# Kernel optimization log

Measured on AMD Instinct MI355X. Metric: run time of the kernel, lower is better.

## Reference

```python
import jax, jax.numpy as jnp
import numpy as np

B, S, IN, H = 16, 1024, 1024, 1024

def setup_inputs() -> dict:
    key = jax.random.key(0)
    k1, k2 = jax.random.split(key)
    x = jax.random.normal(k1, (B, S, IN), dtype=jnp.float32)
    # xavier_uniform with gain sqrt(2) over shape [2H, IN]
    limit = np.sqrt(2.0) * np.sqrt(6.0 / (2 * H + IN))
    W = jax.random.uniform(k2, (2 * H, IN), dtype=jnp.float32, minval=-limit, maxval=limit)
    return {"x": x, "W": W}

def reference(x, W):
    # i = x @ W.T -> [B, S, 2H]; split into key/value pre-activations
    i = jnp.einsum('bsi,oi->bso', x, W)
    ik, iv = jnp.split(i, 2, axis=2)          # each [B, S, H]
    mem0 = jnp.zeros((x.shape[0], H, H), dtype=x.dtype)

    def step(mem, kv):
        ik_t, iv_t = kv                        # [B, H] each
        k = jax.nn.relu(ik_t)
        v = jax.nn.relu(iv_t)
        # Hebbian plasticity rule: delta_mem = key outer val
        mem = mem + jnp.einsum('bk,bv->bkv', k, v)
        return mem, (k, v)

    # scan over time: move seq axis to front
    kv_seq = (jnp.swapaxes(ik, 0, 1), jnp.swapaxes(iv, 0, 1))  # [S, B, H]
    mem, (keys, vals) = jax.lax.scan(step, mem0, kv_seq)
    keys = jnp.swapaxes(keys, 0, 1)            # [B, S, H]
    vals = jnp.swapaxes(vals, 0, 1)
    return mem, keys, vals
```

## Files before the change

### kernel.cpp

```cpp
#include <hip/hip_runtime.h>

#define B_  16
#define S_  1024
#define IN_ 1024
#define H_  1024
#define N1  (2*H_)
#define M1  (B_*S_)
#define K1  IN_
#define XN  (M1*IN_)
#define WN  (N1*IN_)
#define LDG 1024

#define BM  256
#define BN  256
#define BK  64
#define CP  257

typedef __attribute__((ext_vector_type(8))) short  short8;
typedef __attribute__((ext_vector_type(4))) float  floatx4;

__device__ __forceinline__ unsigned short f2bf(float f) {
    unsigned int u = __float_as_uint(f);
    u += 0x7fffu + ((u >> 16) & 1u);
    return (unsigned short)(u >> 16);
}

#define GLDS16(gp, lp) __builtin_amdgcn_global_load_lds(                      \
    (const __attribute__((address_space(1))) void*)(gp),                      \
    (__attribute__((address_space(3))) void*)(lp), 16, 0, 0)

__global__ __launch_bounds__(256) void convert_kernel(
    const float* __restrict__ x, const float* __restrict__ W,
    unsigned short* __restrict__ xb, unsigned short* __restrict__ Wb)
{
    size_t i = ((size_t)blockIdx.x * 256 + threadIdx.x) * 8;
    const float* src;
    unsigned short* dst;
    if (i < (size_t)XN) { src = x + i; dst = xb + i; }
    else                { src = W + (i - XN); dst = Wb + (i - XN); }
    float4 a = *(const float4*)(src);
    float4 b = *(const float4*)(src + 4);
    ushort4 p = { f2bf(a.x), f2bf(a.y), f2bf(a.z), f2bf(a.w) };
    ushort4 q = { f2bf(b.x), f2bf(b.y), f2bf(b.z), f2bf(b.w) };
    *(ushort4*)(dst)     = p;
    *(ushort4*)(dst + 4) = q;
}

__device__ __forceinline__ void stage_unit(
    const unsigned short* Ag, const unsigned short* Bg,
    unsigned short* lbuf, int u, int kt, int wave, int lane)
{
    const unsigned short* src = (u < 2) ? (Ag + (size_t)u * 128 * LDG)
                                        : (Bg + (size_t)(u - 2) * 128 * LDG);
    unsigned short* dstu = lbuf + ((u < 2) ? u * 8192 : 16384 + (u - 2) * 8192);
#pragma unroll
    for (int h = 0; h < 2; ++h) {
        int e   = (wave * 2 + h) * 64 + lane;
        int row = e >> 3, c = e & 7;
        int cs  = c ^ (row & 7);
        GLDS16(src + (size_t)row * LDG + kt + cs * 8, dstu + (wave * 2 + h) * 512);
    }
}

__device__ __forceinline__ void gemm_core(
    const unsigned short* Ag, const unsigned short* Bg,
    unsigned short* lds, floatx4 (&acc)[8][4], int wave, int lane)
{
    const int quad = lane >> 4, r = lane & 15;
    const int wmw  = (wave >> 2) * 128;
    const int wnw  = (wave & 3) * 64;

#pragma unroll
    for (int u = 0; u < 4; ++u) stage_unit(Ag, Bg, lds, u, 0, wave, lane);

    for (int t = 0; t < 16; ++t) {
        unsigned short* bufc = lds + (t & 1) * 32768;
        unsigned short* bufn = lds + ((t + 1) & 1) * 32768;
        const int  ktn = (t + 1) * BK;
        const bool st  = (t < 15);
        __syncthreads();
        const unsigned short* cA = bufc;
        const unsigned short* cB = bufc + 16384;
        short8 bfr[4];
#pragma unroll
        for (int kc = 0; kc < 2; ++kc)
#pragma unroll
        for (int mh = 0; mh < 2; ++mh) {
            const int g = kc * 4 + quad;
            short8 af[4];
#pragma unroll
            for (int i = 0; i < 4; ++i)
                af[i] = *(const short8*)(cA + (wmw + (mh * 4 + i) * 16 + r) * BK
                                            + (g ^ (r & 7)) * 8);
            if (mh == 0) {
#pragma unroll
                for (int j = 0; j < 4; ++j)
                    bfr[j] = *(const short8*)(cB + (wnw + j * 16 + r) * BK
                                                 + (g ^ (r & 7)) * 8);
            }
            if (st) stage_unit(Ag, Bg, bufn, kc * 2 + mh, ktn, wave, lane);
            __builtin_amdgcn_sched_barrier(0);
            __builtin_amdgcn_s_barrier();
            __builtin_amdgcn_s_setprio(1);
#pragma unroll
            for (int i = 0; i < 4; ++i)
#pragma unroll
                for (int j = 0; j < 4; ++j)
                    acc[mh * 4 + i][j] = __builtin_amdgcn_mfma_f32_16x16x32_bf16(
                        af[i], bfr[j], acc[mh * 4 + i][j], 0, 0, 0);
            __builtin_amdgcn_s_setprio(0);
            __builtin_amdgcn_sched_barrier(0);
            if (kc + mh < 2) __builtin_amdgcn_s_barrier();
        }
    }
    __syncthreads();
}

__global__ __launch_bounds__(512, 2) void gemm1_kernel(
    const unsigned short* __restrict__ xb, const unsigned short* __restrict__ Wb,
    float* __restrict__ out,
    unsigned short* __restrict__ kT, unsigned short* __restrict__ vT)
{
    __shared__ unsigned short lds[65536];

    const int tid  = threadIdx.x;
    const int wave = tid >> 6, lane = tid & 63;
    const int quad = lane >> 4, r = lane & 15;
    const int wmw  = (wave >> 2) * 128;
    const int wnw  = (wave & 3) * 64;

    const int L   = blockIdx.x;
    const int xcd = L & 7, s = L >> 3;
    const int mt  = xcd * 8 + (s >> 3);
    const int nt  = s & 7;
    const int m0  = mt * BM, n0 = nt * BN;

    const unsigned short* Ag = xb + (size_t)m0 * K1;
    const unsigned short* Bg = Wb + (size_t)n0 * K1;

    floatx4 acc[8][4] = {};
    gemm_core(Ag, Bg, lds, acc, wave, lane);

    const bool isKeys = (nt < 4);
    float* outKV    = out + (isKeys ? (size_t)M1 * H_ : (size_t)2 * M1 * H_);
    const int ncol0 = isKeys ? n0 : (n0 - 1024);

#pragma unroll
    for (int f = 0; f < 8; ++f)
#pragma unroll
        for (int j = 0; j < 4; ++j)
#pragma unroll
            for (int d = 0; d < 4; ++d) {
                int row_l = wmw + f * 16 + quad * 4 + d;
                int col_l = wnw + j * 16 + r;
                outKV[(size_t)(m0 + row_l) * H_ + ncol0 + col_l] =
                    fmaxf(acc[f][j][d], 0.0f);
            }

    unsigned short* wsT = isKeys ? kT : vT;
    const int b  = m0 >> 10;
    const int s0 = m0 & 1023;
    unsigned short* dstB = wsT + (size_t)b * H_ * S_ + (size_t)ncol0 * S_ + s0;

#pragma unroll
    for (int ch = 0; ch < 2; ++ch) {
        if ((wave >> 2) == ch) {
#pragma unroll
            for (int f = 0; f < 8; ++f)
#pragma unroll
                for (int j = 0; j < 4; ++j)
#pragma unroll
                    for (int d = 0; d < 4; ++d) {
                        int lrow = f * 16 + quad * 4 + d;
                        int col  = wnw + j * 16 + r;
                        lds[lrow * CP + col] = f2bf(fmaxf(acc[f][j][d], 0.0f));
                    }
        }
        __syncthreads();
#pragma unroll
        for (int it = 0; it < 16; ++it) {
            int o   = it * 512 + tid;
            int n_l = o >> 5;
            int m4  = (o & 31) * 4;
            ushort4 v;
            v.x = lds[(m4 + 0) * CP + n_l];
            v.y = lds[(m4 + 1) * CP + n_l];
            v.z = lds[(m4 + 2) * CP + n_l];
            v.w = lds[(m4 + 3) * CP + n_l];
            *(ushort4*)(dstB + (size_t)n_l * S_ + ch * 128 + m4) = v;
        }
        __syncthreads();
    }
}

__global__ __launch_bounds__(512, 2) void gemm2_kernel(
    const unsigned short* __restrict__ kT, const unsigned short* __restrict__ vT,
    float* __restrict__ mem)
{
    __shared__ unsigned short lds[65536];

    const int tid  = threadIdx.x;
    const int wave = tid >> 6, lane = tid & 63;
    const int quad = lane >> 4, r = lane & 15;
    const int wmw  = (wave >> 2) * 128;
    const int wnw  = (wave & 3) * 64;

    const int L   = blockIdx.x;
    const int xcd = L & 7, s = L >> 3;
    const int b   = xcd * 2 + (s >> 4);
    const int tt  = s & 15;
    const int m0  = (tt >> 2) * BM;
    const int n0  = (tt & 3) * BN;

    const unsigned short* Ag = kT + (size_t)b * H_ * S_ + (size_t)m0 * S_;
    const unsigned short* Bg = vT + (size_t)b * H_ * S_ + (size_t)n0 * S_;

    floatx4 acc[8][4] = {};
    gemm_core(Ag, Bg, lds, acc, wave, lane);

    float* outb = mem + (size_t)b * H_ * H_;
#pragma unroll
    for (int f = 0; f < 8; ++f)
#pragma unroll
        for (int j = 0; j < 4; ++j)
#pragma unroll
            for (int d = 0; d < 4; ++d) {
                int row_l = wmw + f * 16 + quad * 4 + d;
                int col_l = wnw + j * 16 + r;
                outb[(size_t)(m0 + row_l) * H_ + n0 + col_l] = acc[f][j][d];
            }
}

extern "C" void kernel_launch(void* const* d_in, const int* in_sizes, int n_in,
                              void* d_out, int out_size, void* d_ws, size_t ws_size,
                              hipStream_t stream) {
    const float* x = (const float*)d_in[0];
    const float* W = (const float*)d_in[1];
    float* out = (float*)d_out;

    unsigned short* xb = (unsigned short*)d_out;
    unsigned short* Wb = xb + (size_t)XN;

    unsigned short* kT = (unsigned short*)d_ws;
    unsigned short* vT = kT + (size_t)B_ * H_ * S_;

    convert_kernel<<<dim3((XN + WN) / 2048), dim3(256), 0, stream>>>(x, W, xb, Wb);

    gemm1_kernel<<<dim3(512), dim3(512), 0, stream>>>(xb, Wb, out, kT, vT);

    gemm2_kernel<<<dim3(256), dim3(512), 0, stream>>>(kT, vT, out);
}
```

Measured before the change: 349.4 us.

## Split GEMM K-tile into halves with vmcnt-gated pipelined staging

Reorganises the LDS tile into two 32-wide K-halves per operand, each with a 4-way XOR swizzle. Synchronisation changes from a full __syncthreads plus extra barriers per iteration to an s_waitcnt vmcnt wait followed by a barrier before each half. The next tile's halves are prefetched while the current half computes, so compute can start as soon as its own half has landed rather than waiting for the whole tile. The risks are weaker bank-conflict avoidance from the narrower swizzle and correctness that depends on exact counts of outstanding loads.

Result: no change. 350.8 us (+0.4%).

```diff
diff --git a/kernel.cpp b/kernel.cpp
--- a/kernel.cpp
+++ b/kernel.cpp
@@ -16,6 +16,10 @@
 #define BK  64
 #define CP  257
 
+#define USZ  8192
+#define ASZ  16384
+#define TBUF 32768
+
 typedef __attribute__((ext_vector_type(8))) short  short8;
 typedef __attribute__((ext_vector_type(4))) float  floatx4;
 
@@ -28,6 +32,10 @@
 #define GLDS16(gp, lp) __builtin_amdgcn_global_load_lds(                      \
     (const __attribute__((address_space(1))) void*)(gp),                      \
     (__attribute__((address_space(3))) void*)(lp), 16, 0, 0)
+
+#define WAITVM(N) { asm volatile("s_waitcnt vmcnt(" #N ")" ::: "memory");     \
+                    __builtin_amdgcn_s_barrier();                             \
+                    __builtin_amdgcn_sched_barrier(0); }
 
 __global__ __launch_bounds__(256) void convert_kernel(
     const float* __restrict__ x, const float* __restrict__ W,
@@ -46,19 +54,50 @@
     *(ushort4*)(dst + 4) = q;
 }
 
-__device__ __forceinline__ void stage_unit(
+__device__ __forceinline__ void stage_u(
     const unsigned short* Ag, const unsigned short* Bg,
-    unsigned short* lbuf, int u, int kt, int wave, int lane)
-{
-    const unsigned short* src = (u < 2) ? (Ag + (size_t)u * 128 * LDG)
-                                        : (Bg + (size_t)(u - 2) * 128 * LDG);
-    unsigned short* dstu = lbuf + ((u < 2) ? u * 8192 : 16384 + (u - 2) * 8192);
+    unsigned short* buf, int op, int kh, int kt, int wave, int lane)
+{
+    const unsigned short* src = op ? Bg : Ag;
+    unsigned short* dst = buf + op * ASZ + kh * USZ;
 #pragma unroll
     for (int h = 0; h < 2; ++h) {
         int e   = (wave * 2 + h) * 64 + lane;
-        int row = e >> 3, c = e & 7;
-        int cs  = c ^ (row & 7);
-        GLDS16(src + (size_t)row * LDG + kt + cs * 8, dstu + (wave * 2 + h) * 512);
+        int row = e >> 2, p = e & 3;
+        int c   = p ^ (row & 3);
+        GLDS16(src + (size_t)row * LDG + kt + kh * 32 + c * 8,
+               dst + (wave * 2 + h) * 512);
+    }
+}
+
+__device__ __forceinline__ void half_tile(
+    const unsigned short* bufc, floatx4 (&acc)[8][4], int kc,
+    const unsigned short* Ag, const unsigned short* Bg,
+    unsigned short* bufn, int ktn, bool st,
+    int wave, int lane, int wmw, int wnw, int quad, int r)
+{
+    const unsigned short* cA = bufc + kc * USZ;
+    const unsigned short* cB = bufc + ASZ + kc * USZ;
+    const int sw = (quad ^ (r & 3)) * 8;
+    short8 bfr[4];
+#pragma unroll
+    for (int j = 0; j < 4; ++j)
+        bfr[j] = *(const short8*)(cB + (wnw + j * 16 + r) * 32 + sw);
+#pragma unroll
+    for (int mh = 0; mh < 2; ++mh) {
+        short8 af[4];
+#pragma unroll
+        for (int i = 0; i < 4; ++i)
+            af[i] = *(const short8*)(cA + (wmw + (mh * 4 + i) * 16 + r) * 32 + sw);
+        if (st) stage_u(Ag, Bg, bufn, mh, kc, ktn, wave, lane);
+        __builtin_amdgcn_s_setprio(1);
+#pragma unroll
+        for (int i = 0; i < 4; ++i)
+#pragma unroll
+            for (int j = 0; j < 4; ++j)
+                acc[mh * 4 + i][j] = __builtin_amdgcn_mfma_f32_16x16x32_bf16(
+                    af[i], bfr[j], acc[mh * 4 + i][j], 0, 0, 0);
+        __builtin_amdgcn_s_setprio(0);
     }
 }
 
@@ -70,48 +109,26 @@
     const int wmw  = (wave >> 2) * 128;
     const int wnw  = (wave & 3) * 64;
 
-#pragma unroll
-    for (int u = 0; u < 4; ++u) stage_unit(Ag, Bg, lds, u, 0, wave, lane);
-
-    for (int t = 0; t < 16; ++t) {
-        unsigned short* bufc = lds + (t & 1) * 32768;
-        unsigned short* bufn = lds + ((t + 1) & 1) * 32768;
-        const int  ktn = (t + 1) * BK;
-        const bool st  = (t < 15);
-        __syncthreads();
-        const unsigned short* cA = bufc;
-        const unsigned short* cB = bufc + 16384;
-        short8 bfr[4];
-#pragma unroll
-        for (int kc = 0; kc < 2; ++kc)
-#pragma unroll
-        for (int mh = 0; mh < 2; ++mh) {
-            const int g = kc * 4 + quad;
-            short8 af[4];
-#pragma unroll
-            for (int i = 0; i < 4; ++i)
-                af[i] = *(const short8*)(cA + (wmw + (mh * 4 + i) * 16 + r) * BK
-                                            + (g ^ (r & 7)) * 8);
-            if (mh == 0) {
-#pragma unroll
-                for (int j = 0; j < 4; ++j)
-                    bfr[j] = *(const short8*)(cB + (wnw + j * 16 + r) * BK
-                                                 + (g ^ (r & 7)) * 8);
-            }
-            if (st) stage_unit(Ag, Bg, bufn, kc * 2 + mh, ktn, wave, lane);
-            __builtin_amdgcn_sched_barrier(0);
-            __builtin_amdgcn_s_barrier();
-            __builtin_amdgcn_s_setprio(1);
-#pragma unroll
-            for (int i = 0; i < 4; ++i)
-#pragma unroll
-                for (int j = 0; j < 4; ++j)
-                    acc[mh * 4 + i][j] = __builtin_amdgcn_mfma_f32_16x16x32_bf16(
-                        af[i], bfr[j], acc[mh * 4 + i][j], 0, 0, 0);
-            __builtin_amdgcn_s_setprio(0);
-            __builtin_amdgcn_sched_barrier(0);
-            if (kc + mh < 2) __builtin_amdgcn_s_barrier();
-        }
+    stage_u(Ag, Bg, lds, 0, 0, 0, wave, lane);
+    stage_u(Ag, Bg, lds, 1, 0, 0, wave, lane);
+    stage_u(Ag, Bg, lds, 0, 1, 0, wave, lane);
+    stage_u(Ag, Bg, lds, 1, 1, 0, wave, lane);
+
+    for (int t = 0; t < 15; ++t) {
+        unsigned short* bufc = lds + (t & 1) * TBUF;
+        unsigned short* bufn = lds + ((t + 1) & 1) * TBUF;
+        const int ktn = (t + 1) * BK;
+        WAITVM(4)
+        half_tile(bufc, acc, 0, Ag, Bg, bufn, ktn, true, wave, lane, wmw, wnw, quad, r);
+        WAITVM(4)
+        half_tile(bufc, acc, 1, Ag, Bg, bufn, ktn, true, wave, lane, wmw, wnw, quad, r);
+    }
+    {
+        unsigned short* bufc = lds + TBUF;
+        WAITVM(4)
+        half_tile(bufc, acc, 0, Ag, Bg, bufc, 0, false, wave, lane, wmw, wnw, quad, r);
+        WAITVM(0)
+        half_tile(bufc, acc, 1, Ag, Bg, bufc, 0, false, wave, lane, wmw, wnw, quad, r);
     }
     __syncthreads();
 }
```

## Shrink GEMM tiles to 128x256 with 3-slot LDS ring and BK=32

Applied to the files above, without the earlier changes.

Both GEMMs switch from 256x256 tiles with BK=64 double buffering to 128x256 tiles with BK=32 and a three-slot LDS ring. Each slot is waited on with explicit vmcnt counters and a single barrier per k-step. Smaller tiles halve accumulator registers and LDS use, aiming for 4 blocks per CU and twice as many workgroups, which improves occupancy and latency hiding. The cost is lower arithmetic intensity per tile and more k-iterations with barrier overhead, and the transpose epilogue now stages the full tile in LDS at once.

New measurement: 365.9 us. 1.05x slower.

```diff
diff --git a/kernel.cpp b/kernel.cpp
--- a/kernel.cpp
+++ b/kernel.cpp
@@ -9,12 +9,12 @@
 #define K1  IN_
 #define XN  (M1*IN_)
 #define WN  (N1*IN_)
-#define LDG 1024
-
-#define BM  256
-#define BN  256
-#define BK  64
-#define CP  257
+
+#define BMr  128
+#define BNr  256
+#define SLOT 12288
+#define RING 36864
+#define CPP  264
 
 typedef __attribute__((ext_vector_type(8))) short  short8;
 typedef __attribute__((ext_vector_type(4))) float  floatx4;
@@ -46,99 +46,88 @@
     *(ushort4*)(dst + 4) = q;
 }
 
-__device__ __forceinline__ void stage_unit(
+__device__ __forceinline__ void stage_ph(
     const unsigned short* Ag, const unsigned short* Bg,
-    unsigned short* lbuf, int u, int kt, int wave, int lane)
-{
-    const unsigned short* src = (u < 2) ? (Ag + (size_t)u * 128 * LDG)
-                                        : (Bg + (size_t)(u - 2) * 128 * LDG);
-    unsigned short* dstu = lbuf + ((u < 2) ? u * 8192 : 16384 + (u - 2) * 8192);
+    unsigned short* slot, int kt, int wave, int lane)
+{
+    {
+        int e   = wave * 64 + lane;
+        int row = e >> 2, p = e & 3, c = p ^ (row & 3);
+        GLDS16(Ag + (size_t)row * 1024 + kt + c * 8, slot + (size_t)e * 8);
+    }
 #pragma unroll
     for (int h = 0; h < 2; ++h) {
-        int e   = (wave * 2 + h) * 64 + lane;
-        int row = e >> 3, c = e & 7;
-        int cs  = c ^ (row & 7);
-        GLDS16(src + (size_t)row * LDG + kt + cs * 8, dstu + (wave * 2 + h) * 512);
+        int e   = wave * 128 + h * 64 + lane;
+        int row = e >> 2, p = e & 3, c = p ^ (row & 3);
+        GLDS16(Bg + (size_t)row * 1024 + kt + c * 8, slot + 4096 + (size_t)e * 8);
     }
 }
 
 __device__ __forceinline__ void gemm_core(
     const unsigned short* Ag, const unsigned short* Bg,
-    unsigned short* lds, floatx4 (&acc)[8][4], int wave, int lane)
+    unsigned short* lds, floatx4 (&acc)[4][4], int wave, int lane)
 {
     const int quad = lane >> 4, r = lane & 15;
-    const int wmw  = (wave >> 2) * 128;
+    const int wmw  = (wave >> 2) * 64;
     const int wnw  = (wave & 3) * 64;
-
-#pragma unroll
-    for (int u = 0; u < 4; ++u) stage_unit(Ag, Bg, lds, u, 0, wave, lane);
-
-    for (int t = 0; t < 16; ++t) {
-        unsigned short* bufc = lds + (t & 1) * 32768;
-        unsigned short* bufn = lds + ((t + 1) & 1) * 32768;
-        const int  ktn = (t + 1) * BK;
-        const bool st  = (t < 15);
-        __syncthreads();
-        const unsigned short* cA = bufc;
-        const unsigned short* cB = bufc + 16384;
-        short8 bfr[4];
-#pragma unroll
-        for (int kc = 0; kc < 2; ++kc)
-#pragma unroll
-        for (int mh = 0; mh < 2; ++mh) {
-            const int g = kc * 4 + quad;
-            short8 af[4];
-#pragma unroll
-            for (int i = 0; i < 4; ++i)
-                af[i] = *(const short8*)(cA + (wmw + (mh * 4 + i) * 16 + r) * BK
-                                            + (g ^ (r & 7)) * 8);
-            if (mh == 0) {
-#pragma unroll
-                for (int j = 0; j < 4; ++j)
-                    bfr[j] = *(const short8*)(cB + (wnw + j * 16 + r) * BK
-                                                 + (g ^ (r & 7)) * 8);
-            }
-            if (st) stage_unit(Ag, Bg, bufn, kc * 2 + mh, ktn, wave, lane);
-            __builtin_amdgcn_sched_barrier(0);
-            __builtin_amdgcn_s_barrier();
-            __builtin_amdgcn_s_setprio(1);
-#pragma unroll
-            for (int i = 0; i < 4; ++i)
-#pragma unroll
-                for (int j = 0; j < 4; ++j)
-                    acc[mh * 4 + i][j] = __builtin_amdgcn_mfma_f32_16x16x32_bf16(
-                        af[i], bfr[j], acc[mh * 4 + i][j], 0, 0, 0);
-            __builtin_amdgcn_s_setprio(0);
-            __builtin_amdgcn_sched_barrier(0);
-            if (kc + mh < 2) __builtin_amdgcn_s_barrier();
-        }
+    const int sw   = (quad ^ (r & 3)) * 8;
+
+    stage_ph(Ag, Bg, lds,         0, wave, lane);
+    stage_ph(Ag, Bg, lds + SLOT, 32, wave, lane);
+
+    unsigned short* slot_c = lds;
+    unsigned short* slot_s = lds + 2 * SLOT;
+    for (int p = 0; p < 32; ++p) {
+        if (p < 31) asm volatile("s_waitcnt vmcnt(3)" ::: "memory");
+        else        asm volatile("s_waitcnt vmcnt(0)" ::: "memory");
+        __builtin_amdgcn_s_barrier();
+        __builtin_amdgcn_sched_barrier(0);
+        if (p < 30) stage_ph(Ag, Bg, slot_s, (p + 2) * 32, wave, lane);
+        short8 fa[4], fb[4];
+#pragma unroll
+        for (int i = 0; i < 4; ++i)
+            fa[i] = *(const short8*)(slot_c + (wmw + i * 16 + r) * 32 + sw);
+#pragma unroll
+        for (int j = 0; j < 4; ++j)
+            fb[j] = *(const short8*)(slot_c + 4096 + (wnw + j * 16 + r) * 32 + sw);
+        __builtin_amdgcn_s_setprio(1);
+#pragma unroll
+        for (int i = 0; i < 4; ++i)
+#pragma unroll
+            for (int j = 0; j < 4; ++j)
+                acc[i][j] = __builtin_amdgcn_mfma_f32_16x16x32_bf16(
+                    fa[i], fb[j], acc[i][j], 0, 0, 0);
+        __builtin_amdgcn_s_setprio(0);
+        __builtin_amdgcn_sched_barrier(0);
+        slot_c += SLOT; if (slot_c == lds + RING) slot_c = lds;
+        slot_s += SLOT; if (slot_s == lds + RING) slot_s = lds;
     }
     __syncthreads();
 }
 
-__global__ __launch_bounds__(512, 2) void gemm1_kernel(
+__global__ __launch_bounds__(512, 4) void gemm1_kernel(
     const unsigned short* __restrict__ xb, const unsigned short* __restrict__ Wb,
     float* __restrict__ out,
     unsigned short* __restrict__ kT, unsigned short* __restrict__ vT)
 {
-    __shared__ unsigned short lds[65536];
+    __shared__ unsigned short lds[RING];
 
     const int tid  = threadIdx.x;
     const int wave = tid >> 6, lane = tid & 63;
     const int quad = lane >> 4, r = lane & 15;
-    const int wmw  = (wave >> 2) * 128;
+    const int wmw  = (wave >> 2) * 64;
     const int wnw  = (wave & 3) * 64;
 
     const int L   = blockIdx.x;
     const int xcd = L & 7, s = L >> 3;
-    const int mt  = xcd * 8 + (s >> 3);
+    const int mt  = xcd * 16 + (s >> 3);
     const int nt  = s & 7;
-    const int m0  = mt * BM, n0 = nt * BN;
+    const int m0  = mt * BMr, n0 = nt * BNr;
 
     const unsigned short* Ag = xb + (size_t)m0 * K1;
     const unsigned short* Bg = Wb + (size_t)n0 * K1;
 
-    floatx4 acc[8][4] = {};
+    floatx4 acc[4][4] = {};
     gemm_core(Ag, Bg, lds, acc, wave, lane);
 
     const bool isKeys = (nt < 4);
@@ -146,88 +135,82 @@
     const int ncol0 = isKeys ? n0 : (n0 - 1024);
 
 #pragma unroll
-    for (int f = 0; f < 8; ++f)
+    for (int i = 0; i < 4; ++i)
 #pragma unroll
         for (int j = 0; j < 4; ++j)
 #pragma unroll
             for (int d = 0; d < 4; ++d) {
-                int row_l = wmw + f * 16 + quad * 4 + d;
+                int row_l = wmw + i * 16 + quad * 4 + d;
                 int col_l = wnw + j * 16 + r;
                 outKV[(size_t)(m0 + row_l) * H_ + ncol0 + col_l] =
-                    fmaxf(acc[f][j][d], 0.0f);
+                    fmaxf(acc[i][j][d], 0.0f);
             }
+
+#pragma unroll
+    for (int i = 0; i < 4; ++i)
+#pragma unroll
+        for (int j = 0; j < 4; ++j)
+#pragma unroll
+            for (int d = 0; d < 4; ++d) {
+                int row_l = wmw + i * 16 + quad * 4 + d;
+                int col_l = wnw + j * 16 + r;
+                lds[row_l * CPP + col_l] = f2bf(fmaxf(acc[i][j][d], 0.0f));
+            }
+    __syncthreads();
 
     unsigned short* wsT = isKeys ? kT : vT;
     const int b  = m0 >> 10;
     const int s0 = m0 & 1023;
     unsigned short* dstB = wsT + (size_t)b * H_ * S_ + (size_t)ncol0 * S_ + s0;
-
-#pragma unroll
-    for (int ch = 0; ch < 2; ++ch) {
-        if ((wave >> 2) == ch) {
-#pragma unroll
-            for (int f = 0; f < 8; ++f)
-#pragma unroll
-                for (int j = 0; j < 4; ++j)
-#pragma unroll
-                    for (int d = 0; d < 4; ++d) {
-                        int lrow = f * 16 + quad * 4 + d;
-                        int col  = wnw + j * 16 + r;
-                        lds[lrow * CP + col] = f2bf(fmaxf(acc[f][j][d], 0.0f));
-                    }
-        }
-        __syncthreads();
-#pragma unroll
-        for (int it = 0; it < 16; ++it) {
-            int o   = it * 512 + tid;
-            int n_l = o >> 5;
-            int m4  = (o & 31) * 4;
-            ushort4 v;
-            v.x = lds[(m4 + 0) * CP + n_l];
-            v.y = lds[(m4 + 1) * CP + n_l];
-            v.z = lds[(m4 + 2) * CP + n_l];
-            v.w = lds[(m4 + 3) * CP + n_l];
-            *(ushort4*)(dstB + (size_t)n_l * S_ + ch * 128 + m4) = v;
-        }
-        __syncthreads();
-    }
-}
-
-__global__ __launch_bounds__(512, 2) void gemm2_kernel(
+#pragma unroll
+    for (int it = 0; it < 16; ++it) {
+        int o   = it * 512 + tid;
+        int n_l = o >> 5;
+        int m4  = (o & 31) * 4;
+        ushort4 v;
+        v.x = lds[(m4 + 0) * CPP + n_l];
+        v.y = lds[(m4 + 1) * CPP + n_l];
+        v.z = lds[(m4 + 2) * CPP + n_l];
+        v.w = lds[(m4 + 3) * CPP + n_l];
+        *(ushort4*)(dstB + (size_t)n_l * S_ + m4) = v;
+    }
+}
+
+__global__ __launch_bounds__(512, 4) void gemm2_kernel(
     const unsigned short* __restrict__ kT, const unsigned short* __restrict__ vT,
     float* __restrict__ mem)
 {
-    __shared__ unsigned short lds[65536];
+    __shared__ unsigned short lds[RING];
 
     const int tid  = threadIdx.x;
     const int wave = tid >> 6, lane = tid & 63;
     const int quad = lane >> 4, r = lane & 15;
-    const int wmw  = (wave >> 2) * 128;
+    const int wmw  = (wave >> 2) * 64;
     const int wnw  = (wave & 3) * 64;
 
     const int L   = blockIdx.x;
     const int xcd = L & 7, s = L >> 3;
-    const int b   = xcd * 2 + (s >> 4);
-    const int tt  = s & 15;
-    const int m0  = (tt >> 2) * BM;
-    const int n0  = (tt & 3) * BN;
+    const int b   = xcd * 2 + (s >> 5);
+    const int tt  = s & 31;
+    const int m0  = (tt >> 2) * BMr;
+    const int n0  = (tt & 3) * BNr;
 
     const unsigned short* Ag = kT + (size_t)b * H_ * S_ + (size_t)m0 * S_;
     const unsigned short* Bg = vT + (size_t)b * H_ * S_ + (size_t)n0 * S_;
 
-    floatx4 acc[8][4] = {};
+    floatx4 acc[4][4] = {};
     gemm_core(Ag, Bg, lds, acc, wave, lane);
 
     float* outb = mem + (size_t)b * H_ * H_;
 #pragma unroll
-    for (int f = 0; f < 8; ++f)
+    for (int i = 0; i < 4; ++i)
 #pragma unroll
         for (int j = 0; j < 4; ++j)
 #pragma unroll
             for (int d = 0; d < 4; ++d) {
-                int row_l = wmw + f * 16 + quad * 4 + d;
+                int row_l = wmw + i * 16 + quad * 4 + d;
                 int col_l = wnw + j * 16 + r;
-                outb[(size_t)(m0 + row_l) * H_ + n0 + col_l] = acc[f][j][d];
+                outb[(size_t)(m0 + row_l) * H_ + n0 + col_l] = acc[i][j][d];
             }
 }
 
@@ -246,7 +229,7 @@
 
     convert_kernel<<<dim3((XN + WN) / 2048), dim3(256), 0, stream>>>(x, W, xb, Wb);
 
-    gemm1_kernel<<<dim3(512), dim3(512), 0, stream>>>(xb, Wb, out, kT, vT);
-
-    gemm2_kernel<<<dim3(256), dim3(512), 0, stream>>>(kT, vT, out);
-}
+    gemm1_kernel<<<dim3(1024), dim3(512), 0, stream>>>(xb, Wb, out, kT, vT);
+
+    gemm2_kernel<<<dim3(512), dim3(512), 0, stream>>>(kT, vT, out);
+}
```
